# Kernel optimization log

Hardware: AMD Instinct MI355X
Metric: run time of the kernel (lower is better)

## Reference

```python
import jax, jax.numpy as jnp
import numpy as np

N, E, C = 50000, 600000, 128
H, O = 4, 32          # heads = C // 32, out_channels = 32, concat -> H*O == C
HO = H * O
EPS_LN = 1e-5


def _lin_init(key, fan_in, shape):
    return jax.random.normal(key, shape, dtype=jnp.float32) * (1.0 / np.sqrt(fan_in))


def setup_inputs() -> dict:
    key = jax.random.key(0)
    ks = jax.random.split(key, 16)
    return {
        "x": jax.random.normal(ks[0], (N, C), dtype=jnp.float32),
        "edge_attr": jax.random.normal(ks[1], (E, C), dtype=jnp.float32),
        "edge_index": jax.random.randint(ks[2], (2, E), 0, N, dtype=jnp.int64),
        # TransformerConv params
        "Wq": _lin_init(ks[3], C, (C, HO)), "bq": jnp.zeros((HO,), jnp.float32),
        "Wk": _lin_init(ks[4], C, (C, HO)), "bk": jnp.zeros((HO,), jnp.float32),
        "Wv": _lin_init(ks[5], C, (C, HO)), "bv": jnp.zeros((HO,), jnp.float32),
        "We": _lin_init(ks[6], C, (C, HO)),                      # lin_edge, no bias
        "Wskip": _lin_init(ks[7], C, (C, HO)), "bskip": jnp.zeros((HO,), jnp.float32),
        "Wbeta": _lin_init(ks[8], 3 * HO, (3 * HO,)),            # lin_beta, no bias
        # graph LayerNorms (affine)
        "g1": jnp.ones((C,), jnp.float32), "be1": jnp.zeros((C,), jnp.float32),
        "g2": jnp.ones((C,), jnp.float32), "be2": jnp.zeros((C,), jnp.float32),
        # FFN
        "W1": _lin_init(ks[9], C, (C, 4 * C)), "bf1": jnp.zeros((4 * C,), jnp.float32),
        "W2": _lin_init(ks[10], 4 * C, (4 * C, C)), "bf2": jnp.zeros((C,), jnp.float32),
    }


def _graph_ln(x, g, b):
    # PyG gnn.LayerNorm mode='graph', batch=None: scalar mean/std over ALL nodes+channels
    xm = x - jnp.mean(x)
    return (xm / (jnp.std(xm) + EPS_LN)) * g + b


def _transformer_conv(x, edge_index, edge_attr, Wq, bq, Wk, bk, Wv, bv, We,
                      Wskip, bskip, Wbeta):
    src, dst = edge_index[0], edge_index[1]   # flow source_to_target: i = dst
    q = (x @ Wq + bq).reshape(N, H, O)
    k = (x @ Wk + bk).reshape(N, H, O)
    v = (x @ Wv + bv).reshape(N, H, O)
    e = (edge_attr @ We).reshape(E, H, O)
    k_j = k[src] + e                           # [E,H,O]
    v_j = v[src] + e                           # [E,H,O]
    alpha = jnp.einsum('ehd,ehd->eh', q[dst], k_j) / np.sqrt(O)   # [E,H]
    # segment softmax over incoming edges of each target node
    m = jax.ops.segment_max(alpha, dst, num_segments=N)           # [N,H]
    a = jnp.exp(alpha - m[dst])
    s = jax.ops.segment_sum(a, dst, num_segments=N)               # [N,H]
    alpha = a / (s[dst] + 1e-16)
    out = jax.ops.segment_sum(alpha[..., None] * v_j, dst, num_segments=N)
    out = out.reshape(N, HO)
    # beta skip connection
    x_r = x @ Wskip + bskip
    beta = jax.nn.sigmoid(jnp.concatenate([out, x_r, out - x_r], axis=-1) @ Wbeta)
    beta = beta[:, None]
    return beta * x_r + (1.0 - beta) * out


def reference(x, edge_attr, edge_index, Wq, bq, Wk, bk, Wv, bv, We, Wskip, bskip,
              Wbeta, g1, be1, g2, be2, W1, bf1, W2, bf2):
    attn = _transformer_conv(x, edge_index, edge_attr, Wq, bq, Wk, bk, Wv, bv,
                             We, Wskip, bskip, Wbeta)
    x = _graph_ln(x + attn, g1, be1)
    ff = jax.nn.gelu(x @ W1 + bf1, approximate=False) @ W2 + bf2  # dropout: eval
    x = _graph_ln(x + ff, g2, be2)
    return x
```

## Files before the change

### kernel.cpp

```cpp
#include <hip/hip_runtime.h>
#include <math.h>

#define NN 50000
#define EE 600000
#define CD 128
#define FD 512
#define NCF 6400000.0

__device__ __forceinline__ float4 ld4(const float* p){ return *(const float4*)p; }

__global__ __launch_bounds__(256) void qkvs_gemm(
    const float* __restrict__ x,
    const float* __restrict__ Wq, const float* __restrict__ bq,
    const float* __restrict__ Wk, const float* __restrict__ bk,
    const float* __restrict__ Wv, const float* __restrict__ bv,
    const float* __restrict__ Wsk, const float* __restrict__ bsk,
    float* __restrict__ oq, float* __restrict__ okk,
    float* __restrict__ ov, float* __restrict__ osk)
{
    __shared__ float ast[32*132];
    __shared__ float bst[32*132];
    const int tid = threadIdx.x;
    const int r0 = blockIdx.x * 128;
    const float* W; const float* bias; float* out;
    switch (blockIdx.y) {
        case 0:  W = Wq;  bias = bq;  out = oq;  break;
        case 1:  W = Wk;  bias = bk;  out = okk; break;
        case 2:  W = Wv;  bias = bv;  out = ov;  break;
        default: W = Wsk; bias = bsk; out = osk; break;
    }
    const int tc = tid & 15, tr = tid >> 4;
    float acc[8][8];
    #pragma unroll
    for (int i = 0; i < 8; ++i)
        #pragma unroll
        for (int j = 0; j < 8; ++j) acc[i][j] = 0.f;

    for (int kc = 0; kc < 4; ++kc) {
        #pragma unroll
        for (int it = 0; it < 4; ++it) {
            int chunk = it*256 + tid;
            int row = chunk >> 3, c4 = chunk & 7;
            float4 g = make_float4(0.f,0.f,0.f,0.f);
            if (r0 + row < NN) g = ld4(&x[(r0+row)*CD + kc*32 + c4*4]);
            ast[(c4*4+0)*132 + row] = g.x;
            ast[(c4*4+1)*132 + row] = g.y;
            ast[(c4*4+2)*132 + row] = g.z;
            ast[(c4*4+3)*132 + row] = g.w;
        }
        #pragma unroll
        for (int it = 0; it < 4; ++it) {
            int chunk = it*256 + tid;
            int kr = chunk >> 5, c4 = chunk & 31;
            *(float4*)&bst[kr*132 + c4*4] = ld4(&W[(kc*32+kr)*CD + c4*4]);
        }
        __syncthreads();
        #pragma unroll
        for (int k = 0; k < 32; ++k) {
            float4 a0 = *(float4*)&ast[k*132 + tr*8];
            float4 a1 = *(float4*)&ast[k*132 + tr*8 + 4];
            float4 b0 = *(float4*)&bst[k*132 + tc*8];
            float4 b1 = *(float4*)&bst[k*132 + tc*8 + 4];
            float ar[8] = {a0.x,a0.y,a0.z,a0.w,a1.x,a1.y,a1.z,a1.w};
            float br[8] = {b0.x,b0.y,b0.z,b0.w,b1.x,b1.y,b1.z,b1.w};
            #pragma unroll
            for (int i = 0; i < 8; ++i)
                #pragma unroll
                for (int j = 0; j < 8; ++j)
                    acc[i][j] += ar[i]*br[j];
        }
        __syncthreads();
    }
    float bcol[8];
    #pragma unroll
    for (int j = 0; j < 8; ++j) bcol[j] = bias[tc*8+j];
    #pragma unroll
    for (int i = 0; i < 8; ++i) {
        int row = r0 + tr*8 + i;
        if (row < NN) {
            float4 o0 = make_float4(acc[i][0]+bcol[0], acc[i][1]+bcol[1],
                                    acc[i][2]+bcol[2], acc[i][3]+bcol[3]);
            float4 o1 = make_float4(acc[i][4]+bcol[4], acc[i][5]+bcol[5],
                                    acc[i][6]+bcol[6], acc[i][7]+bcol[7]);
            *(float4*)&out[row*CD + tc*8]     = o0;
            *(float4*)&out[row*CD + tc*8 + 4] = o1;
        }
    }
}

__global__ __launch_bounds__(256) void hist_kernel(const int* __restrict__ ei, int* __restrict__ cnt)
{
    int j = blockIdx.x*blockDim.x + threadIdx.x;
    if (j < EE) atomicAdd(&cnt[ei[EE + j]], 1);
}

__global__ __launch_bounds__(256) void scan_kernel(int* __restrict__ cnt, int* __restrict__ off)
{
    __shared__ int part[256];
    const int t = threadIdx.x;
    const int nper = (NN + 255) / 256;
    const int lo = t*nper, hi = min(lo + nper, NN);
    int ssum = 0;
    for (int i = lo; i < hi; ++i) ssum += cnt[i];
    part[t] = ssum;
    __syncthreads();
    if (t == 0) {
        int run = 0;
        for (int i = 0; i < 256; ++i) { int tmp = part[i]; part[i] = run; run += tmp; }
    }
    __syncthreads();
    int run = part[t];
    for (int i = lo; i < hi; ++i) {
        int c = cnt[i];
        off[i] = run;
        cnt[i] = run;
        run += c;
    }
    if (hi == NN) off[NN] = run;
}

__global__ __launch_bounds__(256) void scatter_kernel(
    const int* __restrict__ ei, int* __restrict__ cur, int* __restrict__ elist)
{
    int j = blockIdx.x*blockDim.x + threadIdx.x;
    if (j < EE) {
        int pos = atomicAdd(&cur[ei[EE + j]], 1);
        elist[pos] = j;
    }
}

__global__ __launch_bounds__(256) void fused_attn_kernel(
    const int* __restrict__ ei, const int* __restrict__ off, const int* __restrict__ elist,
    const float* __restrict__ ea, const float* __restrict__ q,
    const float* __restrict__ kmat, const float* __restrict__ vmat,
    const float* __restrict__ We, float* __restrict__ oa)
{
    __shared__ float lds[4][640];
    const int w = threadIdx.x >> 6;
    const int l = threadIdx.x & 63;
    const int n = blockIdx.x*4 + w;
    if (n >= NN) return;
    float* qs = &lds[w][0];
    float* ss = &lds[w][128];
    const int hsel = l >> 5;

    float q0 = q[(size_t)n*CD + l];
    float q1 = q[(size_t)n*CD + 64 + l];
    qs[l] = q0;
    qs[64 + l] = q1;

    const float* Wr0 = We + (size_t)l*CD;
    const float* Wr1 = We + (size_t)(64+l)*CD;
    float wq[4][2];
    #pragma unroll
    for (int h = 0; h < 4; ++h) {
        float a0 = 0.f, a1 = 0.f;
        #pragma unroll
        for (int d4 = 0; d4 < 8; ++d4) {
            float4 qv = *(float4*)&qs[h*32 + d4*4];
            float4 w0 = ld4(&Wr0[h*32 + d4*4]);
            float4 w1 = ld4(&Wr1[h*32 + d4*4]);
            a0 += w0.x*qv.x + w0.y*qv.y + w0.z*qv.z + w0.w*qv.w;
            a1 += w1.x*qv.x + w1.y*qv.y + w1.z*qv.z + w1.w*qv.w;
        }
        wq[h][0] = a0; wq[h][1] = a1;
    }

    const int beg = off[n], end = off[n+1];
    const float inv_sqrt_o = 0.17677669529663687f;
    float s00=0,s01=0,s10=0,s11=0,s20=0,s21=0,s30=0,s31=0;
    float av0=0, av1=0, den0=0, den1=0;
    for (int t = beg; t < end; ++t) {
        int eid = elist[t];
        int src = ei[eid];
        float ea0 = ea[(size_t)eid*CD + l];
        float ea1 = ea[(size_t)eid*CD + 64 + l];
        float k0  = kmat[(size_t)src*CD + l];
        float k1  = kmat[(size_t)src*CD + 64 + l];
        float v0  = vmat[(size_t)src*CD + l];
        float v1  = vmat[(size_t)src*CD + 64 + l];
        float p0 = ea0*wq[0][0] + ea1*wq[0][1];
        float p1 = ea0*wq[1][0] + ea1*wq[1][1];
        float p2 = ea0*wq[2][0] + ea1*wq[2][1];
        float p3 = ea0*wq[3][0] + ea1*wq[3][1];
        float qkL = q0*k0;
        float qkH = q1*k1;
        if (hsel == 0) { p0 += qkL; p2 += qkH; }
        else           { p1 += qkL; p3 += qkH; }
        #pragma unroll
        for (int o = 32; o; o >>= 1) {
            p0 += __shfl_xor(p0, o);
            p1 += __shfl_xor(p1, o);
            p2 += __shfl_xor(p2, o);
            p3 += __shfl_xor(p3, o);
        }
        float aH0 = expf(p0 * inv_sqrt_o);
        float aH1 = expf(p1 * inv_sqrt_o);
        float aH2 = expf(p2 * inv_sqrt_o);
        float aH3 = expf(p3 * inv_sqrt_o);
        s00 += aH0*ea0; s01 += aH0*ea1;
        s10 += aH1*ea0; s11 += aH1*ea1;
        s20 += aH2*ea0; s21 += aH2*ea1;
        s30 += aH3*ea0; s31 += aH3*ea1;
        float aL = hsel ? aH1 : aH0;
        float aH = hsel ? aH3 : aH2;
        av0 += aL*v0; av1 += aH*v1;
        den0 += aL;   den1 += aH;
    }

    ss[0*128 + l] = s00;  ss[0*128 + 64 + l] = s01;
    ss[1*128 + l] = s10;  ss[1*128 + 64 + l] = s11;
    ss[2*128 + l] = s20;  ss[2*128 + 64 + l] = s21;
    ss[3*128 + l] = s30;  ss[3*128 + 64 + l] = s31;
    const float* sh0 = &ss[hsel*128];
    const float* sh1 = &ss[(2+hsel)*128];
    float oe0 = 0.f, oe1 = 0.f;
    #pragma unroll 4
    for (int k = 0; k < 128; ++k) {
        oe0 += sh0[k] * We[k*CD + l];
        oe1 += sh1[k] * We[k*CD + 64 + l];
    }
    oa[(size_t)n*CD + l]      = (av0 + oe0) / (den0 + 1e-16f);
    oa[(size_t)n*CD + 64 + l] = (av1 + oe1) / (den1 + 1e-16f);
}

__global__ __launch_bounds__(256) void combine_kernel(
    const float* __restrict__ x, const float* __restrict__ xr,
    const float* __restrict__ oa,
    const float* __restrict__ Wbeta, float* __restrict__ y, double* __restrict__ red)
{
    const int lane = threadIdx.x & 63;
    const int wid = blockIdx.x*4 + (threadIdx.x >> 6);
    const int nw = gridDim.x*4;
    const int c0 = lane, c1 = lane + 64;
    const float wb_o0 = Wbeta[c0],     wb_o1 = Wbeta[c1];
    const float wb_x0 = Wbeta[128+c0], wb_x1 = Wbeta[128+c1];
    const float wb_d0 = Wbeta[256+c0], wb_d1 = Wbeta[256+c1];
    float lsum = 0.f, lsq = 0.f;
    for (int n = wid; n < NN; n += nw) {
        float o0 = oa[n*CD+c0];
        float o1 = oa[n*CD+c1];
        float r0v = xr[n*CD+c0], r1v = xr[n*CD+c1];
        float d = o0*wb_o0 + r0v*wb_x0 + (o0-r0v)*wb_d0
                + o1*wb_o1 + r1v*wb_x1 + (o1-r1v)*wb_d1;
        #pragma unroll
        for (int off = 32; off; off >>= 1) d += __shfl_xor(d, off);
        float beta = 1.0f / (1.0f + expf(-d));
        float y0 = x[n*CD+c0] + beta*r0v + (1.0f-beta)*o0;
        float y1 = x[n*CD+c1] + beta*r1v + (1.0f-beta)*o1;
        y[n*CD+c0] = y0; y[n*CD+c1] = y1;
        lsum += y0 + y1; lsq += y0*y0 + y1*y1;
    }
    #pragma unroll
    for (int off = 32; off; off >>= 1) {
        lsum += __shfl_xor(lsum, off);
        lsq  += __shfl_xor(lsq,  off);
    }
    if (lane == 0) {
        atomicAdd(&red[0], (double)lsum);
        atomicAdd(&red[1], (double)lsq);
    }
}

__global__ __launch_bounds__(256) void ffn1_gemm(
    const float* __restrict__ y, const float* __restrict__ W1, const float* __restrict__ bf1,
    const float* __restrict__ lng, const float* __restrict__ lnb,
    const double* __restrict__ red, float* __restrict__ h)
{
    __shared__ float ast[32*132];
    __shared__ float bst[32*132];
    const int tid = threadIdx.x;
    const int r0 = blockIdx.x * 128;
    const int cb = blockIdx.y;
    double m = red[0] * (1.0/NCF);
    double var = red[1] * (1.0/NCF) - m*m;
    if (var < 0.0) var = 0.0;
    const float mean = (float)m;
    const float scale = (float)(1.0 / (sqrt(var) + 1e-5));
    const int tc = tid & 15, tr = tid >> 4;
    float acc[8][8];
    #pragma unroll
    for (int i = 0; i < 8; ++i)
        #pragma unroll
        for (int j = 0; j < 8; ++j) acc[i][j] = 0.f;

    for (int kc = 0; kc < 4; ++kc) {
        #pragma unroll
        for (int it = 0; it < 4; ++it) {
            int chunk = it*256 + tid;
            int row = chunk >> 3, c4 = chunk & 7;
            float4 g = make_float4(0.f,0.f,0.f,0.f);
            if (r0 + row < NN) g = ld4(&y[(r0+row)*CD + kc*32 + c4*4]);
            int col = kc*32 + c4*4;
            g.x = (g.x - mean)*scale*lng[col+0] + lnb[col+0];
            g.y = (g.y - mean)*scale*lng[col+1] + lnb[col+1];
            g.z = (g.z - mean)*scale*lng[col+2] + lnb[col+2];
            g.w = (g.w - mean)*scale*lng[col+3] + lnb[col+3];
            ast[(c4*4+0)*132 + row] = g.x;
            ast[(c4*4+1)*132 + row] = g.y;
            ast[(c4*4+2)*132 + row] = g.z;
            ast[(c4*4+3)*132 + row] = g.w;
        }
        #pragma unroll
        for (int it = 0; it < 4; ++it) {
            int chunk = it*256 + tid;
            int kr = chunk >> 5, c4 = chunk & 31;
            *(float4*)&bst[kr*132 + c4*4] = ld4(&W1[(size_t)(kc*32+kr)*FD + cb*128 + c4*4]);
        }
        __syncthreads();
        #pragma unroll
        for (int k = 0; k < 32; ++k) {
            float4 a0 = *(float4*)&ast[k*132 + tr*8];
            float4 a1 = *(float4*)&ast[k*132 + tr*8 + 4];
            float4 b0 = *(float4*)&bst[k*132 + tc*8];
            float4 b1 = *(float4*)&bst[k*132 + tc*8 + 4];
            float ar[8] = {a0.x,a0.y,a0.z,a0.w,a1.x,a1.y,a1.z,a1.w};
            float br[8] = {b0.x,b0.y,b0.z,b0.w,b1.x,b1.y,b1.z,b1.w};
            #pragma unroll
            for (int i = 0; i < 8; ++i)
                #pragma unroll
                for (int j = 0; j < 8; ++j)
                    acc[i][j] += ar[i]*br[j];
        }
        __syncthreads();
    }
    float bcol[8];
    #pragma unroll
    for (int j = 0; j < 8; ++j) bcol[j] = bf1[cb*128 + tc*8 + j];
    #pragma unroll
    for (int i = 0; i < 8; ++i) {
        int row = r0 + tr*8 + i;
        if (row < NN) {
            float o[8];
            #pragma unroll
            for (int j = 0; j < 8; ++j) {
                float hv = acc[i][j] + bcol[j];
                o[j] = 0.5f*hv*(1.0f + erff(hv*0.7071067811865476f));
            }
            float4 o0 = make_float4(o[0],o[1],o[2],o[3]);
            float4 o1 = make_float4(o[4],o[5],o[6],o[7]);
            *(float4*)&h[(size_t)row*FD + cb*128 + tc*8]     = o0;
            *(float4*)&h[(size_t)row*FD + cb*128 + tc*8 + 4] = o1;
        }
    }
}

__global__ __launch_bounds__(256) void ffn2_gemm(
    const float* __restrict__ h, const float* __restrict__ W2, const float* __restrict__ bf2,
    const float* __restrict__ y, const float* __restrict__ lng, const float* __restrict__ lnb,
    double* __restrict__ red, float* __restrict__ outz)
{
    __shared__ float ast[32*132];
    __shared__ float bst[32*132];
    const int tid = threadIdx.x;
    const int r0 = blockIdx.x * 128;
    double m = red[0] * (1.0/NCF);
    double var = red[1] * (1.0/NCF) - m*m;
    if (var < 0.0) var = 0.0;
    const float mean = (float)m;
    const float scale = (float)(1.0 / (sqrt(var) + 1e-5));
    const int tc = tid & 15, tr = tid >> 4;
    float acc[8][8];
    #pragma unroll
    for (int i = 0; i < 8; ++i)
        #pragma unroll
        for (int j = 0; j < 8; ++j) acc[i][j] = 0.f;

    for (int kc = 0; kc < 16; ++kc) {
        #pragma unroll
        for (int it = 0; it < 4; ++it) {
            int chunk = it*256 + tid;
            int row = chunk >> 3, c4 = chunk & 7;
            float4 g = make_float4(0.f,0.f,0.f,0.f);
            if (r0 + row < NN) g = ld4(&h[(size_t)(r0+row)*FD + kc*32 + c4*4]);
            ast[(c4*4+0)*132 + row] = g.x;
            ast[(c4*4+1)*132 + row] = g.y;
            ast[(c4*4+2)*132 + row] = g.z;
            ast[(c4*4+3)*132 + row] = g.w;
        }
        #pragma unroll
        for (int it = 0; it < 4; ++it) {
            int chunk = it*256 + tid;
            int kr = chunk >> 5, c4 = chunk & 31;
            *(float4*)&bst[kr*132 + c4*4] = ld4(&W2[(size_t)(kc*32+kr)*CD + c4*4]);
        }
        __syncthreads();
        #pragma unroll
        for (int k = 0; k < 32; ++k) {
            float4 a0 = *(float4*)&ast[k*132 + tr*8];
            float4 a1 = *(float4*)&ast[k*132 + tr*8 + 4];
            float4 b0 = *(float4*)&bst[k*132 + tc*8];
            float4 b1 = *(float4*)&bst[k*132 + tc*8 + 4];
            float ar[8] = {a0.x,a0.y,a0.z,a0.w,a1.x,a1.y,a1.z,a1.w};
            float br[8] = {b0.x,b0.y,b0.z,b0.w,b1.x,b1.y,b1.z,b1.w};
            #pragma unroll
            for (int i = 0; i < 8; ++i)
                #pragma unroll
                for (int j = 0; j < 8; ++j)
                    acc[i][j] += ar[i]*br[j];
        }
        __syncthreads();
    }
    float g1c[8], b1c[8], bfc[8];
    #pragma unroll
    for (int j = 0; j < 8; ++j) {
        int col = tc*8 + j;
        g1c[j] = lng[col]; b1c[j] = lnb[col]; bfc[j] = bf2[col];
    }
    float lsum = 0.f, lsq = 0.f;
    #pragma unroll
    for (int i = 0; i < 8; ++i) {
        int row = r0 + tr*8 + i;
        if (row < NN) {
            float4 ya = ld4(&y[row*CD + tc*8]);
            float4 yb = ld4(&y[row*CD + tc*8 + 4]);
            float yv[8] = {ya.x,ya.y,ya.z,ya.w,yb.x,yb.y,yb.z,yb.w};
            float z[8];
            #pragma unroll
            for (int j = 0; j < 8; ++j) {
                float x1 = (yv[j] - mean)*scale*g1c[j] + b1c[j];
                z[j] = acc[i][j] + bfc[j] + x1;
                lsum += z[j]; lsq += z[j]*z[j];
            }
            float4 z0 = make_float4(z[0],z[1],z[2],z[3]);
            float4 z1 = make_float4(z[4],z[5],z[6],z[7]);
            *(float4*)&outz[row*CD + tc*8]     = z0;
            *(float4*)&outz[row*CD + tc*8 + 4] = z1;
        }
    }
    #pragma unroll
    for (int off = 32; off; off >>= 1) {
        lsum += __shfl_xor(lsum, off);
        lsq  += __shfl_xor(lsq,  off);
    }
    if ((threadIdx.x & 63) == 0) {
        atomicAdd(&red[2], (double)lsum);
        atomicAdd(&red[3], (double)lsq);
    }
}

__global__ __launch_bounds__(256) void ln2_kernel(
    float* __restrict__ z, const float* __restrict__ g2, const float* __restrict__ b2,
    const double* __restrict__ red)
{
    double m = red[2] * (1.0/NCF);
    double var = red[3] * (1.0/NCF) - m*m;
    if (var < 0.0) var = 0.0;
    const float mean = (float)m;
    const float scale = (float)(1.0 / (sqrt(var) + 1e-5));
    const int stride = gridDim.x * blockDim.x;
    for (int i = blockIdx.x*blockDim.x + threadIdx.x; i < NN*32; i += stride) {
        int c4 = (i & 31) * 4;
        float4 zv = *(float4*)&z[(size_t)i*4];
        float4 gv = ld4(&g2[c4]);
        float4 bv = ld4(&b2[c4]);
        zv.x = (zv.x - mean)*scale*gv.x + bv.x;
        zv.y = (zv.y - mean)*scale*gv.y + bv.y;
        zv.z = (zv.z - mean)*scale*gv.z + bv.z;
        zv.w = (zv.w - mean)*scale*gv.w + bv.w;
        *(float4*)&z[(size_t)i*4] = zv;
    }
}

extern "C" void kernel_launch(void* const* d_in, const int* in_sizes, int n_in,
                              void* d_out, int out_size, void* d_ws, size_t ws_size,
                              hipStream_t stream) {
    const float* x     = (const float*)d_in[0];
    const float* ea    = (const float*)d_in[1];
    const int*   ei    = (const int*)d_in[2];
    const float* Wq    = (const float*)d_in[3];
    const float* bq    = (const float*)d_in[4];
    const float* Wk    = (const float*)d_in[5];
    const float* bk    = (const float*)d_in[6];
    const float* Wv    = (const float*)d_in[7];
    const float* bv    = (const float*)d_in[8];
    const float* We    = (const float*)d_in[9];
    const float* Wsk   = (const float*)d_in[10];
    const float* bsk   = (const float*)d_in[11];
    const float* Wbeta = (const float*)d_in[12];
    const float* g1v   = (const float*)d_in[13];
    const float* be1   = (const float*)d_in[14];
    const float* g2v   = (const float*)d_in[15];
    const float* be2   = (const float*)d_in[16];
    const float* W1    = (const float*)d_in[17];
    const float* bf1   = (const float*)d_in[18];
    const float* W2    = (const float*)d_in[19];
    const float* bf2   = (const float*)d_in[20];

    float* wsf = (float*)d_ws;
    float* q    = wsf;
    float* kk   = wsf +  6400000;
    float* vv   = wsf + 12800000;
    float* xr   = wsf + 19200000;
    float* oa   = wsf + 25600000;
    int*   off  = (int*)(wsf + 34400000);
    int*   cur  = off + 50001;
    int*   elist= cur + 50000;
    double* red = (double*)(wsf + 35100056);
    float* y = q;
    float* h = kk;
    float* zout = (float*)d_out;

    (void)hipMemsetAsync(cur, 0, 50000*sizeof(int), stream);
    (void)hipMemsetAsync(red, 0, 4*sizeof(double), stream);

    hist_kernel<<<(EE+255)/256, 256, 0, stream>>>(ei, cur);
    scan_kernel<<<1, 256, 0, stream>>>(cur, off);
    scatter_kernel<<<(EE+255)/256, 256, 0, stream>>>(ei, cur, elist);

    dim3 gA((NN + 127)/128, 4);
    qkvs_gemm<<<gA, 256, 0, stream>>>(x, Wq,bq, Wk,bk, Wv,bv, Wsk,bsk, q, kk, vv, xr);

    fused_attn_kernel<<<(NN + 3)/4, 256, 0, stream>>>(ei, off, elist, ea, q, kk, vv, We, oa);

    combine_kernel<<<1024, 256, 0, stream>>>(x, xr, oa, Wbeta, y, red);

    dim3 gF((NN + 127)/128, 4);
    ffn1_gemm<<<gF, 256, 0, stream>>>(y, W1, bf1, g1v, be1, red, h);

    ffn2_gemm<<<(NN + 127)/128, 256, 0, stream>>>(h, W2, bf2, y, g1v, be1, red, zout);

    ln2_kernel<<<2048, 256, 0, stream>>>(zout, g2v, be2, red);
}
```

Measured before the change: 1.933 ms.

## Split attention into edge-parallel score kernel and node aggregation kernel

The fused per-node attention kernel is split in two. A score kernel processes 16 edges per wavefront, with 4 lanes per edge doing vectorized dot products against LDS-staged q and We·q, and writes the exp scores to a CSR-ordered buffer. A second node kernel reads those scores and accumulates the value and edge-feature sums without any cross-lane shuffle reductions. This removes the serial one-edge-per-iteration full-wave reduction, but it reads edge_attr twice and adds an extra kernel plus a scores buffer round trip.

```diff
diff --git a/kernel.cpp b/kernel.cpp
--- a/kernel.cpp
+++ b/kernel.cpp
@@ -129,91 +129,117 @@
     }
 }
 
-__global__ __launch_bounds__(256) void fused_attn_kernel(
+__global__ __launch_bounds__(256) void attn_score_kernel(
     const int* __restrict__ ei, const int* __restrict__ off, const int* __restrict__ elist,
     const float* __restrict__ ea, const float* __restrict__ q,
-    const float* __restrict__ kmat, const float* __restrict__ vmat,
-    const float* __restrict__ We, float* __restrict__ oa)
-{
-    __shared__ float lds[4][640];
+    const float* __restrict__ kmat, const float* __restrict__ We,
+    float* __restrict__ a4csr)
+{
+    __shared__ float lds[4][720];
     const int w = threadIdx.x >> 6;
     const int l = threadIdx.x & 63;
     const int n = blockIdx.x*4 + w;
     if (n >= NN) return;
     float* qs = &lds[w][0];
-    float* ss = &lds[w][128];
-    const int hsel = l >> 5;
+    float* wq = &lds[w][144];
 
     float q0 = q[(size_t)n*CD + l];
     float q1 = q[(size_t)n*CD + 64 + l];
-    qs[l] = q0;
-    qs[64 + l] = q1;
+    qs[(l>>5)*36 + (l&31)]       = q0;
+    qs[(2+(l>>5))*36 + (l&31)]   = q1;
 
     const float* Wr0 = We + (size_t)l*CD;
     const float* Wr1 = We + (size_t)(64+l)*CD;
-    float wq[4][2];
     #pragma unroll
     for (int h = 0; h < 4; ++h) {
-        float a0 = 0.f, a1 = 0.f;
+        float s0 = 0.f, s1 = 0.f;
         #pragma unroll
         for (int d4 = 0; d4 < 8; ++d4) {
-            float4 qv = *(float4*)&qs[h*32 + d4*4];
+            float4 qv = *(float4*)&qs[h*36 + d4*4];
             float4 w0 = ld4(&Wr0[h*32 + d4*4]);
             float4 w1 = ld4(&Wr1[h*32 + d4*4]);
-            a0 += w0.x*qv.x + w0.y*qv.y + w0.z*qv.z + w0.w*qv.w;
-            a1 += w1.x*qv.x + w1.y*qv.y + w1.z*qv.z + w1.w*qv.w;
-        }
-        wq[h][0] = a0; wq[h][1] = a1;
+            s0 += w0.x*qv.x + w0.y*qv.y + w0.z*qv.z + w0.w*qv.w;
+            s1 += w1.x*qv.x + w1.y*qv.y + w1.z*qv.z + w1.w*qv.w;
+        }
+        wq[h*144 + (l>>5)*36 + (l&31)]     = s0;
+        wq[h*144 + (2+(l>>5))*36 + (l&31)] = s1;
     }
 
     const int beg = off[n], end = off[n+1];
+    const int slot = l >> 2, c = l & 3;
+    const int nr = (end - beg + 15) >> 4;
     const float inv_sqrt_o = 0.17677669529663687f;
-    float s00=0,s01=0,s10=0,s11=0,s20=0,s21=0,s30=0,s31=0;
+    for (int r = 0; r < nr; ++r) {
+        int es = beg + r*16 + slot;
+        bool act = es < end;
+        float pe0=0.f, pe1=0.f, pe2=0.f, pe3=0.f, qk=0.f;
+        if (act) {
+            int eid = elist[es];
+            int sn  = ei[eid];
+            const float* eap = ea   + (size_t)eid*CD + c*32;
+            const float* kp  = kmat + (size_t)sn*CD + c*32;
+            #pragma unroll
+            for (int d4 = 0; d4 < 8; ++d4) {
+                float4 eav = ld4(eap + d4*4);
+                float4 kv  = ld4(kp + d4*4);
+                float4 qv  = *(float4*)&qs[c*36 + d4*4];
+                float4 w0  = *(float4*)&wq[0*144 + c*36 + d4*4];
+                float4 w1  = *(float4*)&wq[1*144 + c*36 + d4*4];
+                float4 w2  = *(float4*)&wq[2*144 + c*36 + d4*4];
+                float4 w3  = *(float4*)&wq[3*144 + c*36 + d4*4];
+                pe0 += eav.x*w0.x + eav.y*w0.y + eav.z*w0.z + eav.w*w0.w;
+                pe1 += eav.x*w1.x + eav.y*w1.y + eav.z*w1.z + eav.w*w1.w;
+                pe2 += eav.x*w2.x + eav.y*w2.y + eav.z*w2.z + eav.w*w2.w;
+                pe3 += eav.x*w3.x + eav.y*w3.y + eav.z*w3.z + eav.w*w3.w;
+                qk  += qv.x*kv.x + qv.y*kv.y + qv.z*kv.z + qv.w*kv.w;
+            }
+        }
+        pe0 += __shfl_xor(pe0, 1);  pe0 += __shfl_xor(pe0, 2);
+        pe1 += __shfl_xor(pe1, 1);  pe1 += __shfl_xor(pe1, 2);
+        pe2 += __shfl_xor(pe2, 1);  pe2 += __shfl_xor(pe2, 2);
+        pe3 += __shfl_xor(pe3, 1);  pe3 += __shfl_xor(pe3, 2);
+        float pe = (c==0) ? pe0 : (c==1) ? pe1 : (c==2) ? pe2 : pe3;
+        if (act) a4csr[(size_t)es*4 + c] = expf((pe + qk) * inv_sqrt_o);
+    }
+}
+
+__global__ __launch_bounds__(256) void node_kernel(
+    const int* __restrict__ ei, const int* __restrict__ off, const int* __restrict__ elist,
+    const float* __restrict__ a4csr, const float* __restrict__ ea,
+    const float* __restrict__ vmat, const float* __restrict__ We,
+    float* __restrict__ oa)
+{
+    __shared__ float s_lds[4][512];
+    const int w = threadIdx.x >> 6;
+    const int l = threadIdx.x & 63;
+    const int n = blockIdx.x * 4 + w;
+    if (n >= NN) return;
+    const int beg = off[n], end = off[n+1];
+    const int hsel = l >> 5;
+    float s0k0=0,s1k0=0,s2k0=0,s3k0=0;
+    float s0k1=0,s1k1=0,s2k1=0,s3k1=0;
     float av0=0, av1=0, den0=0, den1=0;
     for (int t = beg; t < end; ++t) {
         int eid = elist[t];
         int src = ei[eid];
+        float4 aq = ld4(&a4csr[(size_t)t*4]);
         float ea0 = ea[(size_t)eid*CD + l];
         float ea1 = ea[(size_t)eid*CD + 64 + l];
-        float k0  = kmat[(size_t)src*CD + l];
-        float k1  = kmat[(size_t)src*CD + 64 + l];
         float v0  = vmat[(size_t)src*CD + l];
         float v1  = vmat[(size_t)src*CD + 64 + l];
-        float p0 = ea0*wq[0][0] + ea1*wq[0][1];
-        float p1 = ea0*wq[1][0] + ea1*wq[1][1];
-        float p2 = ea0*wq[2][0] + ea1*wq[2][1];
-        float p3 = ea0*wq[3][0] + ea1*wq[3][1];
-        float qkL = q0*k0;
-        float qkH = q1*k1;
-        if (hsel == 0) { p0 += qkL; p2 += qkH; }
-        else           { p1 += qkL; p3 += qkH; }
-        #pragma unroll
-        for (int o = 32; o; o >>= 1) {
-            p0 += __shfl_xor(p0, o);
-            p1 += __shfl_xor(p1, o);
-            p2 += __shfl_xor(p2, o);
-            p3 += __shfl_xor(p3, o);
-        }
-        float aH0 = expf(p0 * inv_sqrt_o);
-        float aH1 = expf(p1 * inv_sqrt_o);
-        float aH2 = expf(p2 * inv_sqrt_o);
-        float aH3 = expf(p3 * inv_sqrt_o);
-        s00 += aH0*ea0; s01 += aH0*ea1;
-        s10 += aH1*ea0; s11 += aH1*ea1;
-        s20 += aH2*ea0; s21 += aH2*ea1;
-        s30 += aH3*ea0; s31 += aH3*ea1;
-        float aL = hsel ? aH1 : aH0;
-        float aH = hsel ? aH3 : aH2;
-        av0 += aL*v0; av1 += aH*v1;
-        den0 += aL;   den1 += aH;
-    }
-
-    ss[0*128 + l] = s00;  ss[0*128 + 64 + l] = s01;
-    ss[1*128 + l] = s10;  ss[1*128 + 64 + l] = s11;
-    ss[2*128 + l] = s20;  ss[2*128 + 64 + l] = s21;
-    ss[3*128 + l] = s30;  ss[3*128 + 64 + l] = s31;
-    const float* sh0 = &ss[hsel*128];
-    const float* sh1 = &ss[(2+hsel)*128];
+        float aH0 = hsel ? aq.y : aq.x;
+        float aH1 = hsel ? aq.w : aq.z;
+        s0k0 += aq.x*ea0; s1k0 += aq.y*ea0; s2k0 += aq.z*ea0; s3k0 += aq.w*ea0;
+        s0k1 += aq.x*ea1; s1k1 += aq.y*ea1; s2k1 += aq.z*ea1; s3k1 += aq.w*ea1;
+        av0 += aH0*v0; av1 += aH1*v1;
+        den0 += aH0;   den1 += aH1;
+    }
+    s_lds[w][0*128 + l] = s0k0;  s_lds[w][0*128 + 64 + l] = s0k1;
+    s_lds[w][1*128 + l] = s1k0;  s_lds[w][1*128 + 64 + l] = s1k1;
+    s_lds[w][2*128 + l] = s2k0;  s_lds[w][2*128 + 64 + l] = s2k1;
+    s_lds[w][3*128 + l] = s3k0;  s_lds[w][3*128 + 64 + l] = s3k1;
+    const float* sh0 = &s_lds[w][hsel*128];
+    const float* sh1 = &s_lds[w][(2+hsel)*128];
     float oe0 = 0.f, oe1 = 0.f;
     #pragma unroll 4
     for (int k = 0; k < 128; ++k) {
@@ -493,6 +519,7 @@
     float* vv   = wsf + 12800000;
     float* xr   = wsf + 19200000;
     float* oa   = wsf + 25600000;
+    float* a4   = wsf + 32000000;
     int*   off  = (int*)(wsf + 34400000);
     int*   cur  = off + 50001;
     int*   elist= cur + 50000;
@@ -511,7 +538,9 @@
     dim3 gA((NN + 127)/128, 4);
     qkvs_gemm<<<gA, 256, 0, stream>>>(x, Wq,bq, Wk,bk, Wv,bv, Wsk,bsk, q, kk, vv, xr);
 
-    fused_attn_kernel<<<(NN + 3)/4, 256, 0, stream>>>(ei, off, elist, ea, q, kk, vv, We, oa);
+    attn_score_kernel<<<(NN + 3)/4, 256, 0, stream>>>(ei, off, elist, ea, q, kk, We, a4);
+
+    node_kernel<<<(NN + 3)/4, 256, 0, stream>>>(ei, off, elist, a4, ea, vv, We, oa);
 
     combine_kernel<<<1024, 256, 0, stream>>>(x, xr, oa, Wbeta, y, red);
 
```

New measurement: 1.802 ms. 1.07x faster.
